# Kernel optimization log

Hardware: AMD Instinct MI355X
Metric: run time of the kernel (lower is better)

Reference implementation:

```python
import jax, jax.numpy as jnp
import numpy as np

B, NG, H, G, T0, T1 = 4096, 3000, 6, 30, 500, 50  # batch, genes, hidden, genes/term, leaf terms, mid terms
EPS = 1e-5  # BatchNorm1d default eps


def _bn(x, gamma, beta):
    # training-mode BatchNorm1d: biased batch stats over the batch axis
    m = x.mean(axis=0)
    v = ((x - m) ** 2).mean(axis=0)
    return gamma * (x - m) / jnp.sqrt(v + EPS) + beta


def setup_inputs() -> dict:
    key = jax.random.key(0)
    ks = iter(jax.random.split(key, 32))
    rn = lambda shape, s=0.05: jax.random.normal(next(ks), shape, dtype=jnp.float32) * s
    return dict(
        cell_features=jax.random.normal(next(ks), (B, NG), dtype=jnp.float32),
        Wdg=rn((T0 + T1 + 1, G, NG)), bdg=rn((T0 + T1 + 1, G)),
        W0=rn((T0, H, G)), b0=rn((T0, H)), gam0=jnp.ones((T0, H), jnp.float32), bet0=jnp.zeros((T0, H), jnp.float32),
        aw0=rn((T0, H)), ab0=rn((T0,)), av0=rn((T0,)), ac0=rn((T0,)),
        W1=rn((T1, H, 10 * H + G)), b1=rn((T1, H)), gam1=jnp.ones((T1, H), jnp.float32), bet1=jnp.zeros((T1, H), jnp.float32),
        aw1=rn((T1, H)), ab1=rn((T1,)), av1=rn((T1,)), ac1=rn((T1,)),
        W2=rn((H, T1 * H + G)), b2=rn((H,)), gam2=jnp.ones((H,), jnp.float32), bet2=jnp.zeros((H,), jnp.float32),
        aw2=rn((H,)), ab2=rn(()), av2=rn(()), ac2=rn(()),
    )


def reference(cell_features, Wdg, bdg,
              W0, b0, gam0, bet0, aw0, ab0, av0, ac0,
              W1, b1, gam1, bet1, aw1, ab1, av1, ac1,
              W2, b2, gam2, bet2, aw2, ab2, av2, ac2):
    # direct_gene_layer for every term: Linear(ngene -> genes_per_term), no activation
    dg = jnp.einsum('bn,tgn->btg', cell_features, Wdg) + bdg  # [B, 551, G]
    # ---- layer 0 (leaves): input = direct gene output only ----
    z0 = jnp.tanh(jnp.einsum('btg,thg->bth', dg[:, :T0], W0) + b0)
    n0 = _bn(z0, gam0, bet0)                                   # [B, T0, H]
    aux0 = jnp.tanh(jnp.einsum('bth,th->bt', n0, aw0) + ab0) * av0 + ac0
    # ---- layer 1: term t's children are leaves [10t, 10t+10); concat children + direct genes ----
    in1 = jnp.concatenate([n0.reshape(B, T1, 10 * H), dg[:, T0:T0 + T1]], axis=-1)  # [B, T1, 90]
    z1 = jnp.tanh(jnp.einsum('bti,thi->bth', in1, W1) + b1)
    n1 = _bn(z1, gam1, bet1)                                   # [B, T1, H]
    aux1 = jnp.tanh(jnp.einsum('bth,th->bt', n1, aw1) + ab1) * av1 + ac1
    # ---- root: children = all mid terms + direct genes ----
    in2 = jnp.concatenate([n1.reshape(B, T1 * H), dg[:, -1]], axis=-1)  # [B, 330]
    z2 = jnp.tanh(in2 @ W2.T + b2)
    n2 = _bn(z2, gam2, bet2)                                   # [B, H]
    aux2 = jnp.tanh(n2 @ aw2 + ab2) * av2 + ac2                # [B]
    # flatten (aux_out_map, term_NN_out_map) into one array for a single comparable output
    aux_all = jnp.concatenate([aux0, aux1, aux2[:, None]], axis=1)              # [B, 551]
    nn_all = jnp.concatenate([n0.reshape(B, -1), n1.reshape(B, -1), n2], axis=1)  # [B, 551*H]
    return jnp.concatenate([aux_all, nn_all], axis=1)          # [B, 3857]
```

## Files before the change

kernel.cpp:

```cpp
#include <hip/hip_runtime.h>
#include <hip/hip_bf16.h>

#define BATCH 4096
#define NGENE 3000
#define HID   6
#define GPT   30
#define T0N   500
#define T1N   50
#define KP    3008
#define MROWS 4608
#define OUTW  3857
#define BNEPS 1e-5f

typedef __attribute__((ext_vector_type(8))) __bf16 bf16x8;
typedef __attribute__((ext_vector_type(4))) float f32x4;
typedef __attribute__((ext_vector_type(8))) unsigned short ushort8;

__device__ __forceinline__ unsigned short f2bf(float f) {
  unsigned int u = __builtin_bit_cast(unsigned int, f);
  u = (u + 0x7fffu + ((u >> 16) & 1u)) >> 16;
  return (unsigned short)u;
}

__device__ __forceinline__ void gload_lds16(const void* g, void* l) {
  __builtin_amdgcn_global_load_lds(
      (const __attribute__((address_space(1))) unsigned int*)g,
      (__attribute__((address_space(3))) unsigned int*)l, 16, 0, 0);
}

__global__ void cast_cell(const float* __restrict__ x, ushort8* __restrict__ y) {
  int idx = blockIdx.x * 256 + threadIdx.x;
  int r = idx / 376, c8 = idx - r * 376;
  int c = c8 * 8;
  ushort8 o = (ushort8)0;
  if (c < NGENE) {
    const float4* p = (const float4*)(x + (size_t)r * NGENE + c);
    float4 a = p[0], b = p[1];
    o[0] = f2bf(a.x); o[1] = f2bf(a.y); o[2] = f2bf(a.z); o[3] = f2bf(a.w);
    o[4] = f2bf(b.x); o[5] = f2bf(b.y); o[6] = f2bf(b.z); o[7] = f2bf(b.w);
  }
  y[idx] = o;
}

__global__ void v0_build(const float* __restrict__ Wdg, const float* __restrict__ W0,
                         unsigned short* __restrict__ abuf) {
  int n = blockIdx.x * 256 + threadIdx.x;
  int t = blockIdx.y;
  if (n >= KP) return;
  bool valid = n < NGENE;
  float x[GPT];
#pragma unroll
  for (int g = 0; g < GPT; ++g)
    x[g] = valid ? Wdg[((size_t)(t * GPT + g)) * NGENE + n] : 0.f;
#pragma unroll
  for (int h = 0; h < HID; ++h) {
    const float* w = W0 + (t * HID + h) * GPT;
    float s = 0.f;
#pragma unroll
    for (int g = 0; g < GPT; ++g) s += x[g] * w[g];
    abuf[((size_t)(t * HID + h)) * KP + n] = valid ? f2bf(s) : (unsigned short)0;
  }
}

__global__ void cast_wdg_mid(const float* __restrict__ w, ushort8* __restrict__ y) {
  int idx = blockIdx.x * 256 + threadIdx.x;
  if (idx >= 1530 * 376) return;
  int r = idx / 376, c8 = idx - r * 376;
  int c = c8 * 8;
  ushort8 o = (ushort8)0;
  if (c < NGENE) {
    const float4* p = (const float4*)(w + (size_t)(15000 + r) * NGENE + c);
    float4 a = p[0], b = p[1];
    o[0] = f2bf(a.x); o[1] = f2bf(a.y); o[2] = f2bf(a.z); o[3] = f2bf(a.w);
    o[4] = f2bf(b.x); o[5] = f2bf(b.y); o[6] = f2bf(b.z); o[7] = f2bf(b.w);
  }
  y[(size_t)(3000 + r) * 376 + c8] = o;
}

__global__ void zero_tail(ushort8* __restrict__ y) {
  int idx = blockIdx.x * 256 + threadIdx.x;
  if (idx < 78 * 376) y[(size_t)4530 * 376 + idx] = (ushort8)0;
}

__global__ void build_bias(const float* __restrict__ bdg, const float* __restrict__ W0,
                           const float* __restrict__ b0, float* __restrict__ bias) {
  int idx = blockIdx.x * 256 + threadIdx.x;
  if (idx >= MROWS) return;
  float v = 0.f;
  if (idx < 3000) {
    int t = idx / HID;
    float s = b0[idx];
#pragma unroll
    for (int g = 0; g < GPT; ++g) s += W0[idx * GPT + g] * bdg[t * GPT + g];
    v = s;
  } else if (idx < 4530) {
    v = bdg[15000 + idx - 3000];
  }
  bias[idx] = v;
}

__global__ __launch_bounds__(256) void gemm_fused(
    const unsigned short* __restrict__ A,
    const unsigned short* __restrict__ Bt,
    const float* __restrict__ bias,
    float* __restrict__ C) {
  __shared__ unsigned short smem[8192];
  const int tid  = threadIdx.x;
  const int wave = tid >> 6, lane = tid & 63;
  const int wm = wave >> 1, wn = wave & 1;
  const int quad = lane >> 4, fr = lane & 15;
  const int m0 = blockIdx.y * 128, n0 = blockIdx.x * 128;
  const int lrow = lane >> 2;
  const int lcol = (lane & 3) * 8;

  f32x4 acc[16] = {};

  for (int kt = 0; kt < KP / 32; ++kt) {
    const int k0 = kt * 32;
#pragma unroll
    for (int q = 0; q < 4; ++q) {
      int chunk = q * 4 + wave;
      const unsigned short* gsrc;
      if (chunk < 8) {
        int row = m0 + chunk * 16 + lrow;
        gsrc = A + (size_t)row * KP + k0 + lcol;
      } else {
        int row = n0 + (chunk - 8) * 16 + lrow;
        gsrc = Bt + (size_t)row * KP + k0 + lcol;
      }
      gload_lds16(gsrc, &smem[chunk * 512]);
    }
    asm volatile("s_waitcnt vmcnt(0)" ::: "memory");
    __syncthreads();

    bf16x8 af[4], bfr[4];
#pragma unroll
    for (int tm = 0; tm < 4; ++tm)
      af[tm] = ((const bf16x8*)smem)[((wm * 64 + tm * 16 + fr) * 32 + quad * 8) >> 3];
#pragma unroll
    for (int tn = 0; tn < 4; ++tn)
      bfr[tn] = ((const bf16x8*)smem)[(4096 + (wn * 64 + tn * 16 + fr) * 32 + quad * 8) >> 3];
#pragma unroll
    for (int tm = 0; tm < 4; ++tm)
#pragma unroll
      for (int tn = 0; tn < 4; ++tn)
        acc[tm * 4 + tn] = __builtin_amdgcn_mfma_f32_16x16x32_bf16(
            af[tm], bfr[tn], acc[tm * 4 + tn], 0, 0, 0);
    __syncthreads();
  }

#pragma unroll
  for (int tm = 0; tm < 4; ++tm) {
#pragma unroll
    for (int tn = 0; tn < 4; ++tn) {
      int n = n0 + wn * 64 + tn * 16 + fr;
#pragma unroll
      for (int r = 0; r < 4; ++r) {
        int m = m0 + wm * 64 + tm * 16 + quad * 4 + r;
        float v = acc[tm * 4 + tn][r] + bias[m];
        if (m < 3000) v = tanhf(v);
        C[(size_t)m * BATCH + n] = v;
      }
    }
  }
}

__global__ void colstatsT(const float* __restrict__ zT, float* __restrict__ st, int ncols) {
  int c = blockIdx.x;
  if (c >= ncols) return;
  const float* p = zT + (size_t)c * BATCH;
  float s = 0.f, q = 0.f;
  for (int i = threadIdx.x; i < BATCH; i += 256) {
    float v = p[i];
    s += v; q += v * v;
  }
#pragma unroll
  for (int off = 32; off > 0; off >>= 1) {
    s += __shfl_down(s, off);
    q += __shfl_down(q, off);
  }
  __shared__ float ls[8];
  int lane = threadIdx.x & 63, w = threadIdx.x >> 6;
  if (lane == 0) { ls[2 * w] = s; ls[2 * w + 1] = q; }
  __syncthreads();
  if (threadIdx.x == 0) {
    st[2 * c]     = ls[0] + ls[2] + ls[4] + ls[6];
    st[2 * c + 1] = ls[1] + ls[3] + ls[5] + ls[7];
  }
}

__global__ void bnfin(const float* __restrict__ st, const float* __restrict__ gam,
                      const float* __restrict__ bet, float* __restrict__ ss, int ncols) {
  int c = blockIdx.x * 256 + threadIdx.x;
  if (c >= ncols) return;
  float m = st[2 * c] * (1.f / BATCH);
  float v = st[2 * c + 1] * (1.f / BATCH) - m * m;
  float sc = gam[c] * rsqrtf(v + BNEPS);
  ss[2 * c] = sc;
  ss[2 * c + 1] = bet[c] - m * sc;
}

__global__ void norm_emit(const float* __restrict__ zT, const float* __restrict__ ss,
                          float* __restrict__ out, int ncols, int outoff) {
  __shared__ float tile[64][65];
  int lane = threadIdx.x & 63, w = threadIdx.x >> 6;
  int c0 = blockIdx.x * 64, b0 = blockIdx.y * 64;
#pragma unroll
  for (int i = 0; i < 16; ++i) {
    int cc = w * 16 + i, c = c0 + cc;
    float n = 0.f;
    if (c < ncols)
      n = zT[(size_t)c * BATCH + b0 + lane] * ss[2 * c] + ss[2 * c + 1];
    tile[cc][lane] = n;
  }
  __syncthreads();
  int c = c0 + lane;
  if (c < ncols) {
#pragma unroll
    for (int i = 0; i < 16; ++i) {
      int rr = w * 16 + i;
      out[(size_t)(b0 + rr) * OUTW + outoff + c] = tile[lane][rr];
    }
  }
}

__global__ void aux_head(const float* __restrict__ zT, const float* __restrict__ ss,
                         const float* __restrict__ aw, const float* __restrict__ ab,
                         const float* __restrict__ av, const float* __restrict__ ac,
                         float* __restrict__ out, int nterm, int auxoff) {
  int lane = threadIdx.x & 63, tg = threadIdx.x >> 6;
  int t = blockIdx.x * 4 + tg;
  if (t >= nterm) return;
  int b = blockIdx.y * 64 + lane;
  float s = ab[t];
#pragma unroll
  for (int h = 0; h < HID; ++h) {
    int c = t * HID + h;
    float n = zT[(size_t)c * BATCH + b] * ss[2 * c] + ss[2 * c + 1];
    s += n * aw[c];
  }
  out[(size_t)b * OUTW + auxoff + t] = tanhf(s) * av[t] + ac[t];
}

__global__ void layer1_zT(const float* __restrict__ C, const float* __restrict__ ss0,
                          const float* __restrict__ W1, const float* __restrict__ b1,
                          float* __restrict__ z1T, float* __restrict__ st) {
  int lane = threadIdx.x & 63, tg = threadIdx.x >> 6;
  int t = blockIdx.x * 4 + tg;
  if (t >= T1N) return;
  int b = blockIdx.y * 64 + lane;
  const float* z0T = C;
  const float* dgm = C + (size_t)3000 * BATCH;
  float x[90];
#pragma unroll
  for (int j = 0; j < 60; ++j) {
    int c = t * 60 + j;
    x[j] = z0T[(size_t)c * BATCH + b] * ss0[2 * c] + ss0[2 * c + 1];
  }
#pragma unroll
  for (int g = 0; g < GPT; ++g)
    x[60 + g] = dgm[(size_t)(t * GPT + g) * BATCH + b];
#pragma unroll
  for (int h = 0; h < HID; ++h) {
    int c = t * HID + h;
    const float* w = W1 + c * 90;
    float s = b1[c];
#pragma unroll
    for (int i = 0; i < 90; ++i) s += x[i] * w[i];
    float z = tanhf(s);
    z1T[(size_t)c * BATCH + b] = z;
    float s1 = z, s2 = z * z;
#pragma unroll
    for (int off = 32; off > 0; off >>= 1) {
      s1 += __shfl_down(s1, off);
      s2 += __shfl_down(s2, off);
    }
    if (lane == 0) {
      atomicAdd(&st[2 * c], s1);
      atomicAdd(&st[2 * c + 1], s2);
    }
  }
}

__global__ void root_zT(const float* __restrict__ C, const float* __restrict__ z1T,
                        const float* __restrict__ ss1, const float* __restrict__ W2,
                        const float* __restrict__ b2, float* __restrict__ z2T,
                        float* __restrict__ st) {
  int b = blockIdx.x * 256 + threadIdx.x;
  int lane = threadIdx.x & 63;
  const float* dgr = C + (size_t)4500 * BATCH;
  float s[HID];
#pragma unroll
  for (int h = 0; h < HID; ++h) s[h] = b2[h];
  for (int c = 0; c < 300; ++c) {
    float n = z1T[(size_t)c * BATCH + b] * ss1[2 * c] + ss1[2 * c + 1];
#pragma unroll
    for (int h = 0; h < HID; ++h) s[h] += n * W2[h * 330 + c];
  }
#pragma unroll
  for (int g = 0; g < GPT; ++g) {
    float d = dgr[(size_t)g * BATCH + b];
#pragma unroll
    for (int h = 0; h < HID; ++h) s[h] += d * W2[h * 330 + 300 + g];
  }
#pragma unroll
  for (int h = 0; h < HID; ++h) {
    float z = tanhf(s[h]);
    z2T[(size_t)h * BATCH + b] = z;
    float s1 = z, s2 = z * z;
#pragma unroll
    for (int off = 32; off > 0; off >>= 1) {
      s1 += __shfl_down(s1, off);
      s2 += __shfl_down(s2, off);
    }
    if (lane == 0) {
      atomicAdd(&st[2 * h], s1);
      atomicAdd(&st[2 * h + 1], s2);
    }
  }
}

__global__ void root_emit(const float* __restrict__ z2T, const float* __restrict__ ss2,
                          const float* __restrict__ aw2, const float* __restrict__ ab2,
                          const float* __restrict__ av2, const float* __restrict__ ac2,
                          float* __restrict__ out) {
  int b = blockIdx.x * 256 + threadIdx.x;
  float s = ab2[0];
#pragma unroll
  for (int h = 0; h < HID; ++h) {
    float n = z2T[(size_t)h * BATCH + b] * ss2[2 * h] + ss2[2 * h + 1];
    out[(size_t)b * OUTW + 3851 + h] = n;
    s += n * aw2[h];
  }
  out[(size_t)b * OUTW + 550] = tanhf(s) * av2[0] + ac2[0];
}

extern "C" void kernel_launch(void* const* d_in, const int* in_sizes, int n_in,
                              void* d_out, int out_size, void* d_ws, size_t ws_size,
                              hipStream_t stream) {
  (void)in_sizes; (void)n_in; (void)out_size; (void)ws_size;
  const float* cell = (const float*)d_in[0];
  const float* Wdg  = (const float*)d_in[1];
  const float* bdg  = (const float*)d_in[2];
  const float* W0   = (const float*)d_in[3];
  const float* b0   = (const float*)d_in[4];
  const float* gam0 = (const float*)d_in[5];
  const float* bet0 = (const float*)d_in[6];
  const float* aw0  = (const float*)d_in[7];
  const float* ab0  = (const float*)d_in[8];
  const float* av0  = (const float*)d_in[9];
  const float* ac0  = (const float*)d_in[10];
  const float* W1   = (const float*)d_in[11];
  const float* b1   = (const float*)d_in[12];
  const float* gam1 = (const float*)d_in[13];
  const float* bet1 = (const float*)d_in[14];
  const float* aw1  = (const float*)d_in[15];
  const float* ab1  = (const float*)d_in[16];
  const float* av1  = (const float*)d_in[17];
  const float* ac1  = (const float*)d_in[18];
  const float* W2   = (const float*)d_in[19];
  const float* b2   = (const float*)d_in[20];
  const float* gam2 = (const float*)d_in[21];
  const float* bet2 = (const float*)d_in[22];
  const float* aw2  = (const float*)d_in[23];
  const float* ab2  = (const float*)d_in[24];
  const float* av2  = (const float*)d_in[25];
  const float* ac2  = (const float*)d_in[26];
  float* out = (float*)d_out;

  char* ws = (char*)d_ws;
  unsigned short* cellb = (unsigned short*)(ws);
  unsigned short* abuf  = (unsigned short*)(ws + 24641536);
  float*          C     = (float*)(ws + 52363264);
  float*          z1T   = (float*)(ws + 127860736);
  float*          z2T   = (float*)(ws + 132775936);
  float*          st    = (float*)(ws + 132874240);
  float*          ssb   = (float*)(ws + 132907008);
  float*          bias  = (float*)(ws + 132939776);
  float* st0 = st,  *st1 = st + 2 * 3000,  *st2 = st + 2 * 3300;
  float* ss0 = ssb, *ss1 = ssb + 2 * 3000, *ss2 = ssb + 2 * 3300;

  hipMemsetAsync(st, 0, 32768, stream);
  cast_cell<<<6016, 256, 0, stream>>>(cell, (ushort8*)cellb);
  v0_build<<<dim3(12, T0N), 256, 0, stream>>>(Wdg, W0, abuf);
  cast_wdg_mid<<<2248, 256, 0, stream>>>(Wdg, (ushort8*)abuf);
  zero_tail<<<115, 256, 0, stream>>>((ushort8*)abuf);
  build_bias<<<18, 256, 0, stream>>>(bdg, W0, b0, bias);

  gemm_fused<<<dim3(32, 36), 256, 0, stream>>>(abuf, cellb, bias, C);

  colstatsT<<<3000, 256, 0, stream>>>(C, st0, 3000);
  bnfin<<<12, 256, 0, stream>>>(st0, gam0, bet0, ss0, 3000);
  norm_emit<<<dim3(47, 64), 256, 0, stream>>>(C, ss0, out, 3000, 551);
  aux_head<<<dim3(125, 64), 256, 0, stream>>>(C, ss0, aw0, ab0, av0, ac0, out, 500, 0);

  layer1_zT<<<dim3(13, 64), 256, 0, stream>>>(C, ss0, W1, b1, z1T, st1);
  bnfin<<<2, 256, 0, stream>>>(st1, gam1, bet1, ss1, 300);
  norm_emit<<<dim3(5, 64), 256, 0, stream>>>(z1T, ss1, out, 300, 3551);
  aux_head<<<dim3(13, 64), 256, 0, stream>>>(z1T, ss1, aw1, ab1, av1, ac1, out, 50, 500);

  root_zT<<<16, 256, 0, stream>>>(C, z1T, ss1, W2, b2, z2T, st2);
  bnfin<<<1, 256, 0, stream>>>(st2, gam2, bet2, ss2, 6);
  root_emit<<<16, 256, 0, stream>>>(z2T, ss2, aw2, ab2, av2, ac2, out);
}
```

Measured before the change: 692.0 us.

## Fuse BN stats into GEMM epilogue and merge small kernels into few launches

Layer-0 BatchNorm sum and sum-of-squares are now accumulated in the GEMM epilogue with shuffle reductions and atomics, so the separate column-stats pass over the 3000x4096 output goes away. The five preparation kernels and the memset become one block-indexed launch. Norm/aux/layer kernels are grouped into three multi-role launches, with BN scale/shift computed inline instead of in a separate finalize kernel. Aux outputs are staged transposed and written through an LDS transpose, which adds an extra buffer pass and redundant per-thread rsqrt work.

```diff
diff --git a/kernel.cpp b/kernel.cpp
--- a/kernel.cpp
+++ b/kernel.cpp
@@ -28,82 +28,95 @@
       (__attribute__((address_space(3))) unsigned int*)l, 16, 0, 0);
 }
 
-__global__ void cast_cell(const float* __restrict__ x, ushort8* __restrict__ y) {
-  int idx = blockIdx.x * 256 + threadIdx.x;
-  int r = idx / 376, c8 = idx - r * 376;
-  int c = c8 * 8;
-  ushort8 o = (ushort8)0;
-  if (c < NGENE) {
-    const float4* p = (const float4*)(x + (size_t)r * NGENE + c);
-    float4 a = p[0], b = p[1];
-    o[0] = f2bf(a.x); o[1] = f2bf(a.y); o[2] = f2bf(a.z); o[3] = f2bf(a.w);
-    o[4] = f2bf(b.x); o[5] = f2bf(b.y); o[6] = f2bf(b.z); o[7] = f2bf(b.w);
-  }
-  y[idx] = o;
-}
-
-__global__ void v0_build(const float* __restrict__ Wdg, const float* __restrict__ W0,
-                         unsigned short* __restrict__ abuf) {
-  int n = blockIdx.x * 256 + threadIdx.x;
-  int t = blockIdx.y;
-  if (n >= KP) return;
-  bool valid = n < NGENE;
-  float x[GPT];
-#pragma unroll
-  for (int g = 0; g < GPT; ++g)
-    x[g] = valid ? Wdg[((size_t)(t * GPT + g)) * NGENE + n] : 0.f;
-#pragma unroll
-  for (int h = 0; h < HID; ++h) {
-    const float* w = W0 + (t * HID + h) * GPT;
-    float s = 0.f;
-#pragma unroll
-    for (int g = 0; g < GPT; ++g) s += x[g] * w[g];
-    abuf[((size_t)(t * HID + h)) * KP + n] = valid ? f2bf(s) : (unsigned short)0;
-  }
-}
-
-__global__ void cast_wdg_mid(const float* __restrict__ w, ushort8* __restrict__ y) {
-  int idx = blockIdx.x * 256 + threadIdx.x;
-  if (idx >= 1530 * 376) return;
-  int r = idx / 376, c8 = idx - r * 376;
-  int c = c8 * 8;
-  ushort8 o = (ushort8)0;
-  if (c < NGENE) {
-    const float4* p = (const float4*)(w + (size_t)(15000 + r) * NGENE + c);
-    float4 a = p[0], b = p[1];
-    o[0] = f2bf(a.x); o[1] = f2bf(a.y); o[2] = f2bf(a.z); o[3] = f2bf(a.w);
-    o[4] = f2bf(b.x); o[5] = f2bf(b.y); o[6] = f2bf(b.z); o[7] = f2bf(b.w);
-  }
-  y[(size_t)(3000 + r) * 376 + c8] = o;
-}
-
-__global__ void zero_tail(ushort8* __restrict__ y) {
-  int idx = blockIdx.x * 256 + threadIdx.x;
-  if (idx < 78 * 376) y[(size_t)4530 * 376 + idx] = (ushort8)0;
-}
-
-__global__ void build_bias(const float* __restrict__ bdg, const float* __restrict__ W0,
-                           const float* __restrict__ b0, float* __restrict__ bias) {
-  int idx = blockIdx.x * 256 + threadIdx.x;
-  if (idx >= MROWS) return;
-  float v = 0.f;
-  if (idx < 3000) {
-    int t = idx / HID;
-    float s = b0[idx];
-#pragma unroll
-    for (int g = 0; g < GPT; ++g) s += W0[idx * GPT + g] * bdg[t * GPT + g];
-    v = s;
-  } else if (idx < 4530) {
-    v = bdg[15000 + idx - 3000];
-  }
-  bias[idx] = v;
+__device__ __forceinline__ void bn_ss(const float* __restrict__ st,
+                                      const float* __restrict__ gam,
+                                      const float* __restrict__ bet,
+                                      int c, float& sc, float& sh) {
+  float m = st[2 * c] * (1.f / BATCH);
+  float v = st[2 * c + 1] * (1.f / BATCH) - m * m;
+  sc = gam[c] * rsqrtf(v + BNEPS);
+  sh = bet[c] - m * sc;
+}
+
+__global__ __launch_bounds__(256) void prep(
+    const float* __restrict__ cell, const float* __restrict__ Wdg,
+    const float* __restrict__ W0, const float* __restrict__ b0,
+    const float* __restrict__ bdg,
+    ushort8* __restrict__ cellb, unsigned short* __restrict__ abuf,
+    float* __restrict__ bias, float* __restrict__ st) {
+  int blk = blockIdx.x, tid = threadIdx.x;
+  if (blk < 6016) {
+    int idx = blk * 256 + tid;
+    int r = idx / 376, c8 = idx - r * 376;
+    int c = c8 * 8;
+    ushort8 o = (ushort8)0;
+    if (c < NGENE) {
+      const float4* p = (const float4*)(cell + (size_t)r * NGENE + c);
+      float4 a = p[0], b = p[1];
+      o[0] = f2bf(a.x); o[1] = f2bf(a.y); o[2] = f2bf(a.z); o[3] = f2bf(a.w);
+      o[4] = f2bf(b.x); o[5] = f2bf(b.y); o[6] = f2bf(b.z); o[7] = f2bf(b.w);
+    }
+    cellb[idx] = o;
+  } else if (blk < 12016) {
+    int bx = blk - 6016;
+    int xb = bx % 12, t = bx / 12;
+    int n = xb * 256 + tid;
+    if (n >= KP) return;
+    bool valid = n < NGENE;
+    float x[GPT];
+#pragma unroll
+    for (int g = 0; g < GPT; ++g)
+      x[g] = valid ? Wdg[((size_t)(t * GPT + g)) * NGENE + n] : 0.f;
+#pragma unroll
+    for (int h = 0; h < HID; ++h) {
+      const float* w = W0 + (t * HID + h) * GPT;
+      float s = 0.f;
+#pragma unroll
+      for (int g = 0; g < GPT; ++g) s += x[g] * w[g];
+      abuf[((size_t)(t * HID + h)) * KP + n] = valid ? f2bf(s) : (unsigned short)0;
+    }
+  } else if (blk < 14264) {
+    int idx = (blk - 12016) * 256 + tid;
+    if (idx >= 1530 * 376) return;
+    int r = idx / 376, c8 = idx - r * 376;
+    int c = c8 * 8;
+    ushort8 o = (ushort8)0;
+    if (c < NGENE) {
+      const float4* p = (const float4*)(Wdg + (size_t)(15000 + r) * NGENE + c);
+      float4 a = p[0], b = p[1];
+      o[0] = f2bf(a.x); o[1] = f2bf(a.y); o[2] = f2bf(a.z); o[3] = f2bf(a.w);
+      o[4] = f2bf(b.x); o[5] = f2bf(b.y); o[6] = f2bf(b.z); o[7] = f2bf(b.w);
+    }
+    ((ushort8*)abuf)[(size_t)(3000 + r) * 376 + c8] = o;
+  } else if (blk < 14379) {
+    int idx = (blk - 14264) * 256 + tid;
+    if (idx < 78 * 376) ((ushort8*)abuf)[(size_t)4530 * 376 + idx] = (ushort8)0;
+  } else if (blk < 14397) {
+    int idx = (blk - 14379) * 256 + tid;
+    if (idx >= MROWS) return;
+    float v = 0.f;
+    if (idx < 3000) {
+      int t = idx / HID;
+      float s = b0[idx];
+#pragma unroll
+      for (int g = 0; g < GPT; ++g) s += W0[idx * GPT + g] * bdg[t * GPT + g];
+      v = s;
+    } else if (idx < 4530) {
+      v = bdg[15000 + idx - 3000];
+    }
+    bias[idx] = v;
+  } else {
+    int idx = (blk - 14397) * 256 + tid;
+    if (idx < 6612) st[idx] = 0.f;
+  }
 }
 
 __global__ __launch_bounds__(256) void gemm_fused(
     const unsigned short* __restrict__ A,
     const unsigned short* __restrict__ Bt,
     const float* __restrict__ bias,
-    float* __restrict__ C) {
+    float* __restrict__ C,
+    float* __restrict__ st0) {
   __shared__ unsigned short smem[8192];
   const int tid  = threadIdx.x;
   const int wave = tid >> 6, lane = tid & 63;
@@ -151,66 +164,55 @@
 
 #pragma unroll
   for (int tm = 0; tm < 4; ++tm) {
+    const int mbase = m0 + wm * 64 + tm * 16 + quad * 4;
+    float s1[4] = {0.f, 0.f, 0.f, 0.f}, s2[4] = {0.f, 0.f, 0.f, 0.f};
 #pragma unroll
     for (int tn = 0; tn < 4; ++tn) {
       int n = n0 + wn * 64 + tn * 16 + fr;
 #pragma unroll
       for (int r = 0; r < 4; ++r) {
-        int m = m0 + wm * 64 + tm * 16 + quad * 4 + r;
+        int m = mbase + r;
         float v = acc[tm * 4 + tn][r] + bias[m];
-        if (m < 3000) v = tanhf(v);
+        if (m < 3000) {
+          v = tanhf(v);
+          s1[r] += v; s2[r] += v * v;
+        }
         C[(size_t)m * BATCH + n] = v;
       }
     }
-  }
-}
-
-__global__ void colstatsT(const float* __restrict__ zT, float* __restrict__ st, int ncols) {
-  int c = blockIdx.x;
-  if (c >= ncols) return;
-  const float* p = zT + (size_t)c * BATCH;
-  float s = 0.f, q = 0.f;
-  for (int i = threadIdx.x; i < BATCH; i += 256) {
-    float v = p[i];
-    s += v; q += v * v;
-  }
-#pragma unroll
-  for (int off = 32; off > 0; off >>= 1) {
-    s += __shfl_down(s, off);
-    q += __shfl_down(q, off);
-  }
-  __shared__ float ls[8];
-  int lane = threadIdx.x & 63, w = threadIdx.x >> 6;
-  if (lane == 0) { ls[2 * w] = s; ls[2 * w + 1] = q; }
-  __syncthreads();
-  if (threadIdx.x == 0) {
-    st[2 * c]     = ls[0] + ls[2] + ls[4] + ls[6];
-    st[2 * c + 1] = ls[1] + ls[3] + ls[5] + ls[7];
-  }
-}
-
-__global__ void bnfin(const float* __restrict__ st, const float* __restrict__ gam,
-                      const float* __restrict__ bet, float* __restrict__ ss, int ncols) {
-  int c = blockIdx.x * 256 + threadIdx.x;
-  if (c >= ncols) return;
-  float m = st[2 * c] * (1.f / BATCH);
-  float v = st[2 * c + 1] * (1.f / BATCH) - m * m;
-  float sc = gam[c] * rsqrtf(v + BNEPS);
-  ss[2 * c] = sc;
-  ss[2 * c + 1] = bet[c] - m * sc;
-}
-
-__global__ void norm_emit(const float* __restrict__ zT, const float* __restrict__ ss,
-                          float* __restrict__ out, int ncols, int outoff) {
+#pragma unroll
+    for (int r = 0; r < 4; ++r) {
+      int m = mbase + r;
+      if (m < 3000) {
+        float a = s1[r], q = s2[r];
+        a += __shfl_xor(a, 1);  q += __shfl_xor(q, 1);
+        a += __shfl_xor(a, 2);  q += __shfl_xor(q, 2);
+        a += __shfl_xor(a, 4);  q += __shfl_xor(q, 4);
+        a += __shfl_xor(a, 8);  q += __shfl_xor(q, 8);
+        if (fr == 0) {
+          atomicAdd(&st0[2 * m], a);
+          atomicAdd(&st0[2 * m + 1], q);
+        }
+      }
+    }
+  }
+}
+
+__device__ void norm_emit_body(const float* __restrict__ zT, const float* __restrict__ st,
+                               const float* __restrict__ gam, const float* __restrict__ bet,
+                               float* __restrict__ out, int ncols, int outoff,
+                               int xb, int yb) {
   __shared__ float tile[64][65];
   int lane = threadIdx.x & 63, w = threadIdx.x >> 6;
-  int c0 = blockIdx.x * 64, b0 = blockIdx.y * 64;
+  int c0 = xb * 64, b0 = yb * 64;
 #pragma unroll
   for (int i = 0; i < 16; ++i) {
     int cc = w * 16 + i, c = c0 + cc;
     float n = 0.f;
-    if (c < ncols)
-      n = zT[(size_t)c * BATCH + b0 + lane] * ss[2 * c] + ss[2 * c + 1];
+    if (c < ncols) {
+      float sc, sh; bn_ss(st, gam, bet, c, sc, sh);
+      n = zT[(size_t)c * BATCH + b0 + lane] * sc + sh;
+    }
     tile[cc][lane] = n;
   }
   __syncthreads();
@@ -224,115 +226,171 @@
   }
 }
 
-__global__ void aux_head(const float* __restrict__ zT, const float* __restrict__ ss,
-                         const float* __restrict__ aw, const float* __restrict__ ab,
-                         const float* __restrict__ av, const float* __restrict__ ac,
-                         float* __restrict__ out, int nterm, int auxoff) {
-  int lane = threadIdx.x & 63, tg = threadIdx.x >> 6;
-  int t = blockIdx.x * 4 + tg;
-  if (t >= nterm) return;
-  int b = blockIdx.y * 64 + lane;
-  float s = ab[t];
-#pragma unroll
-  for (int h = 0; h < HID; ++h) {
-    int c = t * HID + h;
-    float n = zT[(size_t)c * BATCH + b] * ss[2 * c] + ss[2 * c + 1];
-    s += n * aw[c];
-  }
-  out[(size_t)b * OUTW + auxoff + t] = tanhf(s) * av[t] + ac[t];
-}
-
-__global__ void layer1_zT(const float* __restrict__ C, const float* __restrict__ ss0,
-                          const float* __restrict__ W1, const float* __restrict__ b1,
-                          float* __restrict__ z1T, float* __restrict__ st) {
-  int lane = threadIdx.x & 63, tg = threadIdx.x >> 6;
-  int t = blockIdx.x * 4 + tg;
-  if (t >= T1N) return;
-  int b = blockIdx.y * 64 + lane;
-  const float* z0T = C;
-  const float* dgm = C + (size_t)3000 * BATCH;
-  float x[90];
-#pragma unroll
-  for (int j = 0; j < 60; ++j) {
-    int c = t * 60 + j;
-    x[j] = z0T[(size_t)c * BATCH + b] * ss0[2 * c] + ss0[2 * c + 1];
-  }
-#pragma unroll
-  for (int g = 0; g < GPT; ++g)
-    x[60 + g] = dgm[(size_t)(t * GPT + g) * BATCH + b];
-#pragma unroll
-  for (int h = 0; h < HID; ++h) {
-    int c = t * HID + h;
-    const float* w = W1 + c * 90;
-    float s = b1[c];
-#pragma unroll
-    for (int i = 0; i < 90; ++i) s += x[i] * w[i];
-    float z = tanhf(s);
-    z1T[(size_t)c * BATCH + b] = z;
-    float s1 = z, s2 = z * z;
-#pragma unroll
-    for (int off = 32; off > 0; off >>= 1) {
-      s1 += __shfl_down(s1, off);
-      s2 += __shfl_down(s2, off);
-    }
-    if (lane == 0) {
-      atomicAdd(&st[2 * c], s1);
-      atomicAdd(&st[2 * c + 1], s2);
-    }
-  }
-}
-
-__global__ void root_zT(const float* __restrict__ C, const float* __restrict__ z1T,
-                        const float* __restrict__ ss1, const float* __restrict__ W2,
-                        const float* __restrict__ b2, float* __restrict__ z2T,
-                        float* __restrict__ st) {
-  int b = blockIdx.x * 256 + threadIdx.x;
-  int lane = threadIdx.x & 63;
-  const float* dgr = C + (size_t)4500 * BATCH;
-  float s[HID];
-#pragma unroll
-  for (int h = 0; h < HID; ++h) s[h] = b2[h];
-  for (int c = 0; c < 300; ++c) {
-    float n = z1T[(size_t)c * BATCH + b] * ss1[2 * c] + ss1[2 * c + 1];
-#pragma unroll
-    for (int h = 0; h < HID; ++h) s[h] += n * W2[h * 330 + c];
-  }
-#pragma unroll
-  for (int g = 0; g < GPT; ++g) {
-    float d = dgr[(size_t)g * BATCH + b];
-#pragma unroll
-    for (int h = 0; h < HID; ++h) s[h] += d * W2[h * 330 + 300 + g];
-  }
-#pragma unroll
-  for (int h = 0; h < HID; ++h) {
-    float z = tanhf(s[h]);
-    z2T[(size_t)h * BATCH + b] = z;
-    float s1 = z, s2 = z * z;
-#pragma unroll
-    for (int off = 32; off > 0; off >>= 1) {
-      s1 += __shfl_down(s1, off);
-      s2 += __shfl_down(s2, off);
-    }
-    if (lane == 0) {
-      atomicAdd(&st[2 * h], s1);
-      atomicAdd(&st[2 * h + 1], s2);
-    }
-  }
-}
-
-__global__ void root_emit(const float* __restrict__ z2T, const float* __restrict__ ss2,
-                          const float* __restrict__ aw2, const float* __restrict__ ab2,
-                          const float* __restrict__ av2, const float* __restrict__ ac2,
-                          float* __restrict__ out) {
-  int b = blockIdx.x * 256 + threadIdx.x;
-  float s = ab2[0];
-#pragma unroll
-  for (int h = 0; h < HID; ++h) {
-    float n = z2T[(size_t)h * BATCH + b] * ss2[2 * h] + ss2[2 * h + 1];
-    out[(size_t)b * OUTW + 3851 + h] = n;
-    s += n * aw2[h];
-  }
-  out[(size_t)b * OUTW + 550] = tanhf(s) * av2[0] + ac2[0];
+__global__ __launch_bounds__(256) void fused_l1(
+    const float* __restrict__ C, const float* __restrict__ st0,
+    const float* __restrict__ gam0, const float* __restrict__ bet0,
+    const float* __restrict__ aw0, const float* __restrict__ ab0,
+    const float* __restrict__ av0, const float* __restrict__ ac0,
+    const float* __restrict__ W1, const float* __restrict__ b1,
+    float* __restrict__ out, float* __restrict__ auxT,
+    float* __restrict__ z1T, float* __restrict__ st1) {
+  int blk = blockIdx.x;
+  if (blk < 3008) {
+    norm_emit_body(C, st0, gam0, bet0, out, 3000, 551, blk % 47, blk / 47);
+  } else if (blk < 11008) {
+    int b2 = blk - 3008;
+    int lane = threadIdx.x & 63, tg = threadIdx.x >> 6;
+    int t = (b2 % 125) * 4 + tg;
+    int b = (b2 / 125) * 64 + lane;
+    float s = ab0[t];
+#pragma unroll
+    for (int h = 0; h < HID; ++h) {
+      int c = t * HID + h;
+      float sc, sh; bn_ss(st0, gam0, bet0, c, sc, sh);
+      s += (C[(size_t)c * BATCH + b] * sc + sh) * aw0[c];
+    }
+    auxT[(size_t)t * BATCH + b] = tanhf(s) * av0[t] + ac0[t];
+  } else {
+    int b3 = blk - 11008;
+    int lane = threadIdx.x & 63, tg = threadIdx.x >> 6;
+    int t = (b3 % 13) * 4 + tg;
+    if (t >= T1N) return;
+    int b = (b3 / 13) * 64 + lane;
+    const float* dgm = C + (size_t)3000 * BATCH;
+    float x[90];
+#pragma unroll
+    for (int j = 0; j < 60; ++j) {
+      int c = t * 60 + j;
+      float sc, sh; bn_ss(st0, gam0, bet0, c, sc, sh);
+      x[j] = C[(size_t)c * BATCH + b] * sc + sh;
+    }
+#pragma unroll
+    for (int g = 0; g < GPT; ++g)
+      x[60 + g] = dgm[(size_t)(t * GPT + g) * BATCH + b];
+#pragma unroll
+    for (int h = 0; h < HID; ++h) {
+      int c = t * HID + h;
+      const float* w = W1 + c * 90;
+      float s = b1[c];
+#pragma unroll
+      for (int i = 0; i < 90; ++i) s += x[i] * w[i];
+      float z = tanhf(s);
+      z1T[(size_t)c * BATCH + b] = z;
+      float s1 = z, s2 = z * z;
+#pragma unroll
+      for (int off = 32; off > 0; off >>= 1) {
+        s1 += __shfl_down(s1, off);
+        s2 += __shfl_down(s2, off);
+      }
+      if (lane == 0) {
+        atomicAdd(&st1[2 * c], s1);
+        atomicAdd(&st1[2 * c + 1], s2);
+      }
+    }
+  }
+}
+
+__global__ __launch_bounds__(256) void fused_l2(
+    const float* __restrict__ C, const float* __restrict__ z1T,
+    const float* __restrict__ st1,
+    const float* __restrict__ gam1, const float* __restrict__ bet1,
+    const float* __restrict__ aw1, const float* __restrict__ ab1,
+    const float* __restrict__ av1, const float* __restrict__ ac1,
+    const float* __restrict__ W2, const float* __restrict__ b2,
+    float* __restrict__ out, float* __restrict__ auxT,
+    float* __restrict__ z2T, float* __restrict__ st2) {
+  int blk = blockIdx.x;
+  if (blk < 320) {
+    norm_emit_body(z1T, st1, gam1, bet1, out, 300, 3551, blk % 5, blk / 5);
+  } else if (blk < 1152) {
+    int b2 = blk - 320;
+    int lane = threadIdx.x & 63, tg = threadIdx.x >> 6;
+    int t = (b2 % 13) * 4 + tg;
+    if (t >= T1N) return;
+    int b = (b2 / 13) * 64 + lane;
+    float s = ab1[t];
+#pragma unroll
+    for (int h = 0; h < HID; ++h) {
+      int c = t * HID + h;
+      float sc, sh; bn_ss(st1, gam1, bet1, c, sc, sh);
+      s += (z1T[(size_t)c * BATCH + b] * sc + sh) * aw1[c];
+    }
+    auxT[(size_t)(T0N + t) * BATCH + b] = tanhf(s) * av1[t] + ac1[t];
+  } else {
+    int b = (blk - 1152) * 256 + threadIdx.x;
+    int lane = threadIdx.x & 63;
+    const float* dgr = C + (size_t)4500 * BATCH;
+    float s[HID];
+#pragma unroll
+    for (int h = 0; h < HID; ++h) s[h] = b2[h];
+    for (int c = 0; c < 300; ++c) {
+      float sc, sh; bn_ss(st1, gam1, bet1, c, sc, sh);
+      float n = z1T[(size_t)c * BATCH + b] * sc + sh;
+#pragma unroll
+      for (int h = 0; h < HID; ++h) s[h] += n * W2[h * 330 + c];
+    }
+#pragma unroll
+    for (int g = 0; g < GPT; ++g) {
+      float d = dgr[(size_t)g * BATCH + b];
+#pragma unroll
+      for (int h = 0; h < HID; ++h) s[h] += d * W2[h * 330 + 300 + g];
+    }
+#pragma unroll
+    for (int h = 0; h < HID; ++h) {
+      float z = tanhf(s[h]);
+      z2T[(size_t)h * BATCH + b] = z;
+      float s1 = z, s2 = z * z;
+#pragma unroll
+      for (int off = 32; off > 0; off >>= 1) {
+        s1 += __shfl_down(s1, off);
+        s2 += __shfl_down(s2, off);
+      }
+      if (lane == 0) {
+        atomicAdd(&st2[2 * h], s1);
+        atomicAdd(&st2[2 * h + 1], s2);
+      }
+    }
+  }
+}
+
+__global__ __launch_bounds__(256) void fused_fin(
+    const float* __restrict__ auxT, const float* __restrict__ z2T,
+    const float* __restrict__ st2,
+    const float* __restrict__ gam2, const float* __restrict__ bet2,
+    const float* __restrict__ aw2, const float* __restrict__ ab2,
+    const float* __restrict__ av2, const float* __restrict__ ac2,
+    float* __restrict__ out) {
+  int blk = blockIdx.x;
+  if (blk < 576) {
+    __shared__ float tile[64][65];
+    int lane = threadIdx.x & 63, w = threadIdx.x >> 6;
+    int c0 = (blk % 9) * 64, b0 = (blk / 9) * 64;
+#pragma unroll
+    for (int i = 0; i < 16; ++i) {
+      int cc = w * 16 + i, c = c0 + cc;
+      tile[cc][lane] = (c < 550) ? auxT[(size_t)c * BATCH + b0 + lane] : 0.f;
+    }
+    __syncthreads();
+    int c = c0 + lane;
+    if (c < 550) {
+#pragma unroll
+      for (int i = 0; i < 16; ++i) {
+        int rr = w * 16 + i;
+        out[(size_t)(b0 + rr) * OUTW + c] = tile[lane][rr];
+      }
+    }
+  } else {
+    int b = (blk - 576) * 256 + threadIdx.x;
+    float s = ab2[0];
+#pragma unroll
+    for (int h = 0; h < HID; ++h) {
+      float sc, sh; bn_ss(st2, gam2, bet2, h, sc, sh);
+      float n = z2T[(size_t)h * BATCH + b] * sc + sh;
+      out[(size_t)b * OUTW + 3851 + h] = n;
+      s += n * aw2[h];
+    }
+    out[(size_t)b * OUTW + 550] = tanhf(s) * av2[0] + ac2[0];
+  }
 }
 
 extern "C" void kernel_launch(void* const* d_in, const int* in_sizes, int n_in,
@@ -375,31 +433,17 @@
   float*          z1T   = (float*)(ws + 127860736);
   float*          z2T   = (float*)(ws + 132775936);
   float*          st    = (float*)(ws + 132874240);
-  float*          ssb   = (float*)(ws + 132907008);
-  float*          bias  = (float*)(ws + 132939776);
-  float* st0 = st,  *st1 = st + 2 * 3000,  *st2 = st + 2 * 3300;
-  float* ss0 = ssb, *ss1 = ssb + 2 * 3000, *ss2 = ssb + 2 * 3300;
-
-  hipMemsetAsync(st, 0, 32768, stream);
-  cast_cell<<<6016, 256, 0, stream>>>(cell, (ushort8*)cellb);
-  v0_build<<<dim3(12, T0N), 256, 0, stream>>>(Wdg, W0, abuf);
-  cast_wdg_mid<<<2248, 256, 0, stream>>>(Wdg, (ushort8*)abuf);
-  zero_tail<<<115, 256, 0, stream>>>((ushort8*)abuf);
-  build_bias<<<18, 256, 0, stream>>>(bdg, W0, b0, bias);
-
-  gemm_fused<<<dim3(32, 36), 256, 0, stream>>>(abuf, cellb, bias, C);
-
-  colstatsT<<<3000, 256, 0, stream>>>(C, st0, 3000);
-  bnfin<<<12, 256, 0, stream>>>(st0, gam0, bet0, ss0, 3000);
-  norm_emit<<<dim3(47, 64), 256, 0, stream>>>(C, ss0, out, 3000, 551);
-  aux_head<<<dim3(125, 64), 256, 0, stream>>>(C, ss0, aw0, ab0, av0, ac0, out, 500, 0);
-
-  layer1_zT<<<dim3(13, 64), 256, 0, stream>>>(C, ss0, W1, b1, z1T, st1);
-  bnfin<<<2, 256, 0, stream>>>(st1, gam1, bet1, ss1, 300);
-  norm_emit<<<dim3(5, 64), 256, 0, stream>>>(z1T, ss1, out, 300, 3551);
-  aux_head<<<dim3(13, 64), 256, 0, stream>>>(z1T, ss1, aw1, ab1, av1, ac1, out, 50, 500);
-
-  root_zT<<<16, 256, 0, stream>>>(C, z1T, ss1, W2, b2, z2T, st2);
-  bnfin<<<1, 256, 0, stream>>>(st2, gam2, bet2, ss2, 6);
-  root_emit<<<16, 256, 0, stream>>>(z2T, ss2, aw2, ab2, av2, ac2, out);
-}
+  float*          bias  = (float*)(ws + 132907008);
+  float*          auxT  = (float*)(ws + 132925440);
+  float* st0 = st, *st1 = st + 2 * 3000, *st2 = st + 2 * 3300;
+
+  prep<<<14423, 256, 0, stream>>>(cell, Wdg, W0, b0, bdg,
+                                  (ushort8*)cellb, abuf, bias, st);
+  gemm_fused<<<dim3(32, 36), 256, 0, stream>>>(abuf, cellb, bias, C, st0);
+  fused_l1<<<11840, 256, 0, stream>>>(C, st0, gam0, bet0, aw0, ab0, av0, ac0,
+                                      W1, b1, out, auxT, z1T, st1);
+  fused_l2<<<1168, 256, 0, stream>>>(C, z1T, st1, gam1, bet1, aw1, ab1, av1, ac1,
+                                     W2, b2, out, auxT, z2T, st2);
+  fused_fin<<<592, 256, 0, stream>>>(auxT, z2T, st2, gam2, bet2, aw2, ab2, av2, ac2,
+                                     out);
+}
```

New measurement: 699.4 us. Within noise of the previous version (+1.1%).
